# Kernel optimization log

Measured on AMD Instinct MI355X. Metric: run time of the kernel, lower is better.

The kernel has to match this reference:

```python
import jax, jax.numpy as jnp
import numpy as np

N = 10000
E = 160000
D = 512
EPS = 1e-5


def _lin_params(key, out_d, in_d, bias=True):
    k1, k2 = jax.random.split(key)
    s = 1.0 / np.sqrt(in_d)
    W = jax.random.uniform(k1, (out_d, in_d), jnp.float32, -s, s)
    if bias:
        b = jax.random.uniform(k2, (out_d,), jnp.float32, -s, s)
        return W, b
    return (W,)


def setup_inputs() -> dict:
    key = jax.random.key(0)
    ks = jax.random.split(key, 16)
    inp = {
        "x": jax.random.normal(ks[0], (N, D), jnp.float32),
        "edge_index": jax.random.randint(ks[1], (2, E), 0, N, jnp.int64),
    }
    ki = 2
    for l in range(3):
        Wp, bp = _lin_params(ks[ki], D, D); ki += 1
        Wl, bl = _lin_params(ks[ki], D, D); ki += 1
        (Wr,) = _lin_params(ks[ki], D, D, bias=False); ki += 1
        inp[f"Wp{l}"] = Wp; inp[f"bp{l}"] = bp
        inp[f"Wl{l}"] = Wl; inp[f"bl{l}"] = bl
        inp[f"Wr{l}"] = Wr
        if l < 2:  # ReLU+LayerNorm between convs
            inp[f"g{l}"] = jnp.ones((D,), jnp.float32)
            inp[f"be{l}"] = jnp.zeros((D,), jnp.float32)
    return inp


def _sage_conv(x, src, dst, Wp, bp, Wl, bl, Wr):
    # PyG SAGEConv with project=True: project+ReLU messages, mean-aggregate, lin_l + lin_r(root)
    h = jax.nn.relu(x @ Wp.T + bp)                      # [N, D] projected messages
    agg = jax.ops.segment_sum(h[src], dst, num_segments=N)   # gather + scatter-add
    cnt = jax.ops.segment_sum(jnp.ones((src.shape[0],), x.dtype), dst, num_segments=N)
    agg = agg / jnp.maximum(cnt, 1.0)[:, None]          # mean over incoming edges
    return agg @ Wl.T + bl + x @ Wr.T


def _relu_ln(x, g, b):
    x = jax.nn.relu(x)
    mu = jnp.mean(x, axis=-1, keepdims=True)
    var = jnp.mean(jnp.square(x - mu), axis=-1, keepdims=True)
    return (x - mu) * jax.lax.rsqrt(var + EPS) * g + b


def reference(x, edge_index,
              Wp0, bp0, Wl0, bl0, Wr0, g0, be0,
              Wp1, bp1, Wl1, bl1, Wr1, g1, be1,
              Wp2, bp2, Wl2, bl2, Wr2):
    src, dst = edge_index[0], edge_index[1]
    x = _sage_conv(x, src, dst, Wp0, bp0, Wl0, bl0, Wr0)
    x = _relu_ln(x, g0, be0)
    x = _sage_conv(x, src, dst, Wp1, bp1, Wl1, bl1, Wr1)
    x = _relu_ln(x, g1, be1)
    x = _sage_conv(x, src, dst, Wp2, bp2, Wl2, bl2, Wr2)
    return x
```

## Files before the change

### kernel.cpp

```cpp
#include <hip/hip_runtime.h>
#include <cstdint>

#define D 512
#define TM 128
#define TN 128
#define BK 32
#define CAP 64

typedef unsigned short u16;
typedef __bf16 bf16x8 __attribute__((ext_vector_type(8)));
typedef float f32x4 __attribute__((ext_vector_type(4)));

__device__ __forceinline__ float bf2f(u16 u) {
    unsigned int x = ((unsigned int)u) << 16;
    return __builtin_bit_cast(float, x);
}
__device__ __forceinline__ u16 f2bf(float f) {
    unsigned int x = __builtin_bit_cast(unsigned int, f);
    x += 0x7fffu + ((x >> 16) & 1u);
    return (u16)(x >> 16);
}

__device__ __forceinline__ void gload16(const u16* g, u16* l) {
    __builtin_amdgcn_global_load_lds(
        (const __attribute__((address_space(1))) void*)(uintptr_t)g,
        (__attribute__((address_space(3))) void*)(unsigned int)(uintptr_t)l,
        16, 0, 0);
}

__device__ __forceinline__ bool is_bf16(const u16* xraw) {
    int lane = threadIdx.x & 63;
    u16 u = xraw[2 * lane];
    int e = (u >> 7) & 0xFF;
    unsigned long long b = __ballot(e >= 110 && e <= 129);
    return __popcll(b) >= 32;
}
__device__ __forceinline__ bool is_i64(const int* eraw) {
    int lane = threadIdx.x & 63;
    unsigned long long b = __ballot(eraw[2 * lane + 1] == 0);
    return __popcll(b) >= 32;
}

__global__ __launch_bounds__(256) void convert_x(
    const void* __restrict__ src, u16* __restrict__ out)
{
    bool bf = is_bf16((const u16*)src);
    int i = (blockIdx.x * 256 + threadIdx.x) * 8;
    if (bf) {
        *(uint4*)(out + i) = *(const uint4*)((const u16*)src + i);
    } else {
        const float* f = (const float*)src + i;
        float4 a = *(const float4*)f;
        float4 b = *(const float4*)(f + 4);
        u16 r[8] = {f2bf(a.x), f2bf(a.y), f2bf(a.z), f2bf(a.w),
                    f2bf(b.x), f2bf(b.y), f2bf(b.z), f2bf(b.w)};
        *(uint4*)(out + i) = *(uint4*)r;
    }
}

struct Ptrs9  { const void* p[9];  };
struct Ptrs10 { const void* p[10]; };

__global__ __launch_bounds__(256) void convert_wb(
    Ptrs9 s, Ptrs10 v, u16* __restrict__ wout, float* __restrict__ vout,
    const u16* __restrict__ xraw)
{
    bool bf = is_bf16(xraw);
    int m = blockIdx.y;
    if (m < 9) {
        const void* src = s.p[m];
        u16* o = wout + (size_t)m * D * D;
        int i = (blockIdx.x * 256 + threadIdx.x) * 8;
        if (bf) {
            *(uint4*)(o + i) = *(const uint4*)((const u16*)src + i);
        } else {
            const float* f = (const float*)src + i;
            float4 a = *(const float4*)f;
            float4 b = *(const float4*)(f + 4);
            u16 r[8] = {f2bf(a.x), f2bf(a.y), f2bf(a.z), f2bf(a.w),
                        f2bf(b.x), f2bf(b.y), f2bf(b.z), f2bf(b.w)};
            *(uint4*)(o + i) = *(uint4*)r;
        }
    } else if (blockIdx.x == 0) {
        for (int b = 0; b < 10; b++) {
            const void* src = v.p[b];
            for (int j = threadIdx.x * 2; j < threadIdx.x * 2 + 2; j++) {
                float val = bf ? bf2f(((const u16*)src)[j]) : ((const float*)src)[j];
                vout[b * 512 + j] = val;
            }
        }
    }
}

__global__ void build_bucket(const int* __restrict__ eraw,
                             int* __restrict__ cnt, u16* __restrict__ bucket,
                             int E, int Nn)
{
    bool i64 = is_i64(eraw);
    int e = blockIdx.x * 256 + threadIdx.x;
    if (e < E) {
        int s, d;
        if (i64) { s = eraw[2 * e]; d = eraw[2 * (E + e)]; }
        else     { s = eraw[e];     d = eraw[E + e]; }
        s = min(max(s, 0), Nn - 1);
        d = min(max(d, 0), Nn - 1);
        int p = atomicAdd(&cnt[d], 1);
        if (p < CAP) bucket[(size_t)d * CAP + p] = (u16)s;
    }
}

template <int NPASS, bool RELU, bool FINAL>
__global__ __launch_bounds__(256) void gemm_bt(
    const u16* __restrict__ A0, const u16* __restrict__ B0,
    const u16* __restrict__ A1, const u16* __restrict__ B1,
    const float* __restrict__ bias, void* __restrict__ Cout,
    const u16* __restrict__ xraw, int M)
{
    __shared__ __align__(16) u16 sA[TM * BK];
    __shared__ __align__(16) u16 sB[TN * BK];

    const int t    = threadIdx.x;
    const int m0   = blockIdx.x * TM;
    const int n0   = blockIdx.y * TN;
    const int wave = t >> 6, lane = t & 63;
    const int wm   = wave >> 1, wn = wave & 1;
    const int lrow = lane & 15, quad = lane >> 4;

    const bool out_bf16 = FINAL ? is_bf16(xraw) : true;

    f32x4 acc[4][4];
#pragma unroll
    for (int i = 0; i < 4; i++)
#pragma unroll
        for (int j = 0; j < 4; j++)
#pragma unroll
            for (int r = 0; r < 4; r++) acc[i][j][r] = 0.f;

    const int cA  = (t & 3) * 8;
    const int rA0 = min(m0 + (t >> 2),      M - 1);
    const int rA1 = min(m0 + 64 + (t >> 2), M - 1);
    const int rB0 = n0 + (t >> 2);
    const int rB1 = n0 + 64 + (t >> 2);

#pragma unroll 1
    for (int p = 0; p < NPASS; p++) {
        const u16* A = p ? A1 : A0;
        const u16* B = p ? B1 : B0;
        const u16* gA0 = A + (size_t)rA0 * D + cA;
        const u16* gA1 = A + (size_t)rA1 * D + cA;
        const u16* gB0 = B + (size_t)rB0 * D + cA;
        const u16* gB1 = B + (size_t)rB1 * D + cA;

#pragma unroll 1
        for (int k0 = 0; k0 < D; k0 += BK) {
            gload16(gA0 + k0, &sA[(size_t)t * 8]);
            gload16(gA1 + k0, &sA[(size_t)(t + 256) * 8]);
            gload16(gB0 + k0, &sB[(size_t)t * 8]);
            gload16(gB1 + k0, &sB[(size_t)(t + 256) * 8]);
            __syncthreads();

            bf16x8 af[4], bfr[4];
#pragma unroll
            for (int mi = 0; mi < 4; mi++)
                af[mi] = *(const bf16x8*)&sA[(wm * 64 + mi * 16 + lrow) * BK + quad * 8];
#pragma unroll
            for (int ni = 0; ni < 4; ni++)
                bfr[ni] = *(const bf16x8*)&sB[(wn * 64 + ni * 16 + lrow) * BK + quad * 8];
#pragma unroll
            for (int mi = 0; mi < 4; mi++)
#pragma unroll
                for (int ni = 0; ni < 4; ni++)
                    acc[mi][ni] = __builtin_amdgcn_mfma_f32_16x16x32_bf16(
                        af[mi], bfr[ni], acc[mi][ni], 0, 0, 0);
            __syncthreads();
        }
    }

#pragma unroll
    for (int ni = 0; ni < 4; ni++) {
        int col = n0 + wn * 64 + ni * 16 + lrow;
        float bv = bias[col];
#pragma unroll
        for (int mi = 0; mi < 4; mi++) {
            int row0 = m0 + wm * 64 + mi * 16 + quad * 4;
#pragma unroll
            for (int r = 0; r < 4; r++) {
                int row = row0 + r;
                if (row < M) {
                    float v = acc[mi][ni][r] + bv;
                    if (RELU) v = fmaxf(v, 0.f);
                    if (!FINAL || out_bf16)
                        ((u16*)Cout)[(size_t)row * D + col] = f2bf(v);
                    else
                        ((float*)Cout)[(size_t)row * D + col] = v;
                }
            }
        }
    }
}

__global__ __launch_bounds__(256) void aggregate(
    const u16* __restrict__ h, const int* __restrict__ cnt,
    const u16* __restrict__ bucket, u16* __restrict__ agg, int M)
{
    const int w = threadIdx.x >> 6, lane = threadIdx.x & 63;
    const int n = blockIdx.x * 4 + w;

    __shared__ u16 sidx[4][CAP];
    int deg = 0, dd = 0;
    if (n < M) {
        deg = cnt[n];
        dd  = min(deg, CAP);
        if (lane < dd) sidx[w][lane] = bucket[(size_t)n * CAP + lane];
    }
    __syncthreads();
    if (n >= M) return;

    float a[8] = {0.f, 0.f, 0.f, 0.f, 0.f, 0.f, 0.f, 0.f};
    int i = 0;
    for (; i + 4 <= dd; i += 4) {
        uint4 v0 = *(const uint4*)(h + (size_t)sidx[w][i]     * D + lane * 8);
        uint4 v1 = *(const uint4*)(h + (size_t)sidx[w][i + 1] * D + lane * 8);
        uint4 v2 = *(const uint4*)(h + (size_t)sidx[w][i + 2] * D + lane * 8);
        uint4 v3 = *(const uint4*)(h + (size_t)sidx[w][i + 3] * D + lane * 8);
        const unsigned int* u0 = (const unsigned int*)&v0;
        const unsigned int* u1 = (const unsigned int*)&v1;
        const unsigned int* u2 = (const unsigned int*)&v2;
        const unsigned int* u3 = (const unsigned int*)&v3;
#pragma unroll
        for (int j = 0; j < 4; j++) {
            a[2 * j]     += bf2f((u16)(u0[j] & 0xffffu)) + bf2f((u16)(u1[j] & 0xffffu))
                          + bf2f((u16)(u2[j] & 0xffffu)) + bf2f((u16)(u3[j] & 0xffffu));
            a[2 * j + 1] += bf2f((u16)(u0[j] >> 16)) + bf2f((u16)(u1[j] >> 16))
                          + bf2f((u16)(u2[j] >> 16)) + bf2f((u16)(u3[j] >> 16));
        }
    }
    for (; i < dd; i++) {
        uint4 v0 = *(const uint4*)(h + (size_t)sidx[w][i] * D + lane * 8);
        const unsigned int* u0 = (const unsigned int*)&v0;
#pragma unroll
        for (int j = 0; j < 4; j++) {
            a[2 * j]     += bf2f((u16)(u0[j] & 0xffffu));
            a[2 * j + 1] += bf2f((u16)(u0[j] >> 16));
        }
    }

    float inv = 1.f / fmaxf((float)deg, 1.f);
    u16 r[8];
#pragma unroll
    for (int j = 0; j < 8; j++) r[j] = f2bf(a[j] * inv);
    *(uint4*)(agg + (size_t)n * D + lane * 8) = *(uint4*)r;
}

__global__ __launch_bounds__(256) void relu_ln(
    const u16* __restrict__ y, const float* __restrict__ g, const float* __restrict__ be,
    u16* __restrict__ out, int M)
{
    const int row  = blockIdx.x * 4 + (threadIdx.x >> 6);
    const int lane = threadIdx.x & 63;
    if (row >= M) return;

    typedef short s16x8 __attribute__((ext_vector_type(8)));
    s16x8 v = *(const s16x8*)(y + (size_t)row * D + lane * 8);
    float f[8], s = 0.f, s2 = 0.f;
#pragma unroll
    for (int i = 0; i < 8; i++) {
        float x = bf2f((u16)v[i]);
        x = fmaxf(x, 0.f);
        f[i] = x; s += x; s2 += x * x;
    }
#pragma unroll
    for (int off = 32; off >= 1; off >>= 1) {
        s  += __shfl_xor(s, off);
        s2 += __shfl_xor(s2, off);
    }
    float mean = s * (1.f / 512.f);
    float var  = s2 * (1.f / 512.f) - mean * mean;
    float rstd = rsqrtf(var + 1e-5f);

    s16x8 res;
#pragma unroll
    for (int i = 0; i < 8; i++) {
        float o = (f[i] - mean) * rstd * g[lane * 8 + i] + be[lane * 8 + i];
        res[i] = (short)f2bf(o);
    }
    *(s16x8*)(out + (size_t)row * D + lane * 8) = res;
}

extern "C" void kernel_launch(void* const* d_in, const int* in_sizes, int n_in,
                              void* d_out, int out_size, void* d_ws, size_t ws_size,
                              hipStream_t stream)
{
    const int M = in_sizes[0] / D;
    const int E = in_sizes[1] / 2;
    const void* xraw = d_in[0];
    const int*  eraw = (const int*)d_in[1];

    const void *Wp[3], *bp[3], *Wl[3], *bl[3], *Wr[3], *g[2], *be[2];
    int idx = 2;
    for (int l = 0; l < 3; l++) {
        Wp[l] = d_in[idx++]; bp[l] = d_in[idx++];
        Wl[l] = d_in[idx++]; bl[l] = d_in[idx++];
        Wr[l] = d_in[idx++];
        if (l < 2) { g[l] = d_in[idx++]; be[l] = d_in[idx++]; }
    }

    char* w = (char*)d_ws;
    auto alloc = [&](size_t bytes) { void* p = w; w += (bytes + 255) & ~(size_t)255; return p; };
    u16*   xb     = (u16*)  alloc((size_t)M * D * 2);
    u16*   h      = (u16*)  alloc((size_t)M * D * 2);
    u16*   agg    = (u16*)  alloc((size_t)M * D * 2);
    u16*   Wb     = (u16*)  alloc((size_t)9 * D * D * 2);
    float* vecf   = (float*)alloc((size_t)10 * 512 * 4);
    int*   cnt    = (int*)  alloc((size_t)M * 4);
    u16*   bucket = (u16*)  alloc((size_t)M * CAP * 2);

    convert_x<<<dim3(M * D / (256 * 8)), dim3(256), 0, stream>>>(xraw, xb);

    Ptrs9 mats;
    const void* morder[9] = {Wp[0], Wl[0], Wr[0], Wp[1], Wl[1], Wr[1], Wp[2], Wl[2], Wr[2]};
    for (int i = 0; i < 9; i++) mats.p[i] = morder[i];
    Ptrs10 vecs;
    const void* vorder[10] = {bp[0], bl[0], g[0], be[0], bp[1], bl[1], g[1], be[1], bp[2], bl[2]};
    for (int i = 0; i < 10; i++) vecs.p[i] = vorder[i];
    convert_wb<<<dim3(D * D / (256 * 8), 10), dim3(256), 0, stream>>>(
        mats, vecs, Wb, vecf, (const u16*)xraw);

    hipMemsetAsync(cnt, 0, (size_t)M * 4, stream);
    build_bucket<<<dim3((E + 255) / 256), dim3(256), 0, stream>>>(eraw, cnt, bucket, E, M);

    const u16* WM[9]; for (int i = 0; i < 9; i++) WM[i] = Wb + (size_t)i * D * D;
    const float* VB[10]; for (int i = 0; i < 10; i++) VB[i] = vecf + (size_t)i * 512;

    u16* yb = (u16*)d_out;
    dim3 gg((M + TM - 1) / TM, D / TN);
    const u16* xin = xb;
    for (int l = 0; l < 3; l++) {
        gemm_bt<1, true, false><<<gg, dim3(256), 0, stream>>>(
            xin, WM[l * 3 + 0], xin, WM[l * 3 + 0], VB[l * 4 + 0], h, (const u16*)xraw, M);
        aggregate<<<dim3((M + 3) / 4), dim3(256), 0, stream>>>(h, cnt, bucket, agg, M);
        if (l < 2) {
            gemm_bt<2, false, false><<<gg, dim3(256), 0, stream>>>(
                agg, WM[l * 3 + 1], xin, WM[l * 3 + 2], VB[l * 4 + 1], yb, (const u16*)xraw, M);
            relu_ln<<<dim3((M + 3) / 4), dim3(256), 0, stream>>>(
                yb, VB[l * 4 + 2], VB[l * 4 + 3], xb, M);
            xin = xb;
        } else {
            gemm_bt<2, false, true><<<gg, dim3(256), 0, stream>>>(
                agg, WM[l * 3 + 1], xin, WM[l * 3 + 2], VB[l * 4 + 1], d_out, (const u16*)xraw, M);
        }
    }
}
```

Baseline: 381.0 us.

## Fuse whole pipeline into one persistent kernel with grid barriers

Replaces the separate conversion, bucket-build, GEMM, aggregate and LayerNorm launches with a single persistent kernel that uses a software grid barrier between phases. The GEMM also switches from direct global-to-LDS loads to register-prefetched double buffering, and the aggregation keeps neighbor indices in registers and broadcasts them with shuffles instead of staging them in shared memory. The intent is to remove launch overhead and inter-kernel gaps. In exchange, each barrier costs global atomics and spinning, and the grid size is fixed by the GEMM tile count. Correctness relies on every block being co-resident, which the launch does not guarantee, so the barrier can deadlock.

```diff
diff --git a/kernel.cpp b/kernel.cpp
--- a/kernel.cpp
+++ b/kernel.cpp
@@ -19,13 +19,6 @@
     unsigned int x = __builtin_bit_cast(unsigned int, f);
     x += 0x7fffu + ((x >> 16) & 1u);
     return (u16)(x >> 16);
-}
-
-__device__ __forceinline__ void gload16(const u16* g, u16* l) {
-    __builtin_amdgcn_global_load_lds(
-        (const __attribute__((address_space(1))) void*)(uintptr_t)g,
-        (__attribute__((address_space(3))) void*)(unsigned int)(uintptr_t)l,
-        16, 0, 0);
 }
 
 __device__ __forceinline__ bool is_bf16(const u16* xraw) {
@@ -41,92 +34,94 @@
     return __popcll(b) >= 32;
 }
 
-__global__ __launch_bounds__(256) void convert_x(
-    const void* __restrict__ src, u16* __restrict__ out)
+struct Args {
+    const u16* xraw; const int* eraw;
+    const void* W[9];
+    const void* V[10];
+    u16* xb; u16* h; u16* agg; u16* Wb; float* vecf;
+    int* cnt; u16* bucket; int* bar;
+    void* dout;
+    int M, E, NGRP;
+};
+
+__device__ __forceinline__ void grid_sync(int* cnt, int* gen, int nb) {
+    __syncthreads();
+    if (threadIdx.x == 0) {
+        int g0 = __hip_atomic_load(gen, __ATOMIC_RELAXED, __HIP_MEMORY_SCOPE_AGENT);
+        __threadfence();
+        int prev = __hip_atomic_fetch_add(cnt, 1, __ATOMIC_RELAXED, __HIP_MEMORY_SCOPE_AGENT);
+        if (prev == nb - 1) {
+            __hip_atomic_store(cnt, 0, __ATOMIC_RELAXED, __HIP_MEMORY_SCOPE_AGENT);
+            __hip_atomic_fetch_add(gen, 1, __ATOMIC_RELAXED, __HIP_MEMORY_SCOPE_AGENT);
+        } else {
+            while (__hip_atomic_load(gen, __ATOMIC_RELAXED, __HIP_MEMORY_SCOPE_AGENT) == g0)
+                __builtin_amdgcn_s_sleep(2);
+        }
+        __threadfence();
+    }
+    __syncthreads();
+}
+
+__device__ void phase0(const Args& a, bool bf, bool i64) {
+    const int gt = blockIdx.x * 256 + threadIdx.x;
+    const int gs = gridDim.x * 256;
+
+    const int nx = a.M * D / 8;
+    for (int i = gt; i < nx; i += gs) {
+        if (bf) {
+            *(uint4*)(a.xb + i * 8) = *(const uint4*)(a.xraw + i * 8);
+        } else {
+            const float* f = (const float*)a.xraw + i * 8;
+            float4 p = *(const float4*)f, q = *(const float4*)(f + 4);
+            u16 r[8] = {f2bf(p.x), f2bf(p.y), f2bf(p.z), f2bf(p.w),
+                        f2bf(q.x), f2bf(q.y), f2bf(q.z), f2bf(q.w)};
+            *(uint4*)(a.xb + i * 8) = *(uint4*)r;
+        }
+    }
+    for (int i = gt; i < 9 * 32768; i += gs) {
+        int m = i >> 15, j = i & 32767;
+        const void* src = a.W[m];
+        u16* o = a.Wb + (size_t)m * D * D + j * 8;
+        if (bf) {
+            *(uint4*)o = *(const uint4*)((const u16*)src + j * 8);
+        } else {
+            const float* f = (const float*)src + j * 8;
+            float4 p = *(const float4*)f, q = *(const float4*)(f + 4);
+            u16 r[8] = {f2bf(p.x), f2bf(p.y), f2bf(p.z), f2bf(p.w),
+                        f2bf(q.x), f2bf(q.y), f2bf(q.z), f2bf(q.w)};
+            *(uint4*)o = *(uint4*)r;
+        }
+    }
+    if (blockIdx.x < 10) {
+        const void* src = a.V[blockIdx.x];
+        for (int j = threadIdx.x * 2; j < threadIdx.x * 2 + 2; j++) {
+            a.vecf[blockIdx.x * 512 + j] =
+                bf ? bf2f(((const u16*)src)[j]) : ((const float*)src)[j];
+        }
+    }
+    for (int e = gt; e < a.E; e += gs) {
+        int s, d;
+        if (i64) { s = a.eraw[2 * e]; d = a.eraw[2 * (a.E + e)]; }
+        else     { s = a.eraw[e];     d = a.eraw[a.E + e]; }
+        s = min(max(s, 0), a.M - 1);
+        d = min(max(d, 0), a.M - 1);
+        int p = atomicAdd(&a.cnt[d], 1);
+        if (p < CAP) a.bucket[(size_t)d * CAP + p] = (u16)s;
+    }
+}
+
+template <int NPASS, bool RELU, bool FINAL>
+__device__ void gemm_tile(const u16* __restrict__ A0, const u16* __restrict__ B0,
+                          const u16* __restrict__ A1, const u16* __restrict__ B1,
+                          const float* __restrict__ bias, void* __restrict__ Cout,
+                          int M, bool out_bf16, u16* sA, u16* sB)
 {
-    bool bf = is_bf16((const u16*)src);
-    int i = (blockIdx.x * 256 + threadIdx.x) * 8;
-    if (bf) {
-        *(uint4*)(out + i) = *(const uint4*)((const u16*)src + i);
-    } else {
-        const float* f = (const float*)src + i;
-        float4 a = *(const float4*)f;
-        float4 b = *(const float4*)(f + 4);
-        u16 r[8] = {f2bf(a.x), f2bf(a.y), f2bf(a.z), f2bf(a.w),
-                    f2bf(b.x), f2bf(b.y), f2bf(b.z), f2bf(b.w)};
-        *(uint4*)(out + i) = *(uint4*)r;
-    }
-}
-
-struct Ptrs9  { const void* p[9];  };
-struct Ptrs10 { const void* p[10]; };
-
-__global__ __launch_bounds__(256) void convert_wb(
-    Ptrs9 s, Ptrs10 v, u16* __restrict__ wout, float* __restrict__ vout,
-    const u16* __restrict__ xraw)
-{
-    bool bf = is_bf16(xraw);
-    int m = blockIdx.y;
-    if (m < 9) {
-        const void* src = s.p[m];
-        u16* o = wout + (size_t)m * D * D;
-        int i = (blockIdx.x * 256 + threadIdx.x) * 8;
-        if (bf) {
-            *(uint4*)(o + i) = *(const uint4*)((const u16*)src + i);
-        } else {
-            const float* f = (const float*)src + i;
-            float4 a = *(const float4*)f;
-            float4 b = *(const float4*)(f + 4);
-            u16 r[8] = {f2bf(a.x), f2bf(a.y), f2bf(a.z), f2bf(a.w),
-                        f2bf(b.x), f2bf(b.y), f2bf(b.z), f2bf(b.w)};
-            *(uint4*)(o + i) = *(uint4*)r;
-        }
-    } else if (blockIdx.x == 0) {
-        for (int b = 0; b < 10; b++) {
-            const void* src = v.p[b];
-            for (int j = threadIdx.x * 2; j < threadIdx.x * 2 + 2; j++) {
-                float val = bf ? bf2f(((const u16*)src)[j]) : ((const float*)src)[j];
-                vout[b * 512 + j] = val;
-            }
-        }
-    }
-}
-
-__global__ void build_bucket(const int* __restrict__ eraw,
-                             int* __restrict__ cnt, u16* __restrict__ bucket,
-                             int E, int Nn)
-{
-    bool i64 = is_i64(eraw);
-    int e = blockIdx.x * 256 + threadIdx.x;
-    if (e < E) {
-        int s, d;
-        if (i64) { s = eraw[2 * e]; d = eraw[2 * (E + e)]; }
-        else     { s = eraw[e];     d = eraw[E + e]; }
-        s = min(max(s, 0), Nn - 1);
-        d = min(max(d, 0), Nn - 1);
-        int p = atomicAdd(&cnt[d], 1);
-        if (p < CAP) bucket[(size_t)d * CAP + p] = (u16)s;
-    }
-}
-
-template <int NPASS, bool RELU, bool FINAL>
-__global__ __launch_bounds__(256) void gemm_bt(
-    const u16* __restrict__ A0, const u16* __restrict__ B0,
-    const u16* __restrict__ A1, const u16* __restrict__ B1,
-    const float* __restrict__ bias, void* __restrict__ Cout,
-    const u16* __restrict__ xraw, int M)
-{
-    __shared__ __align__(16) u16 sA[TM * BK];
-    __shared__ __align__(16) u16 sB[TN * BK];
-
     const int t    = threadIdx.x;
-    const int m0   = blockIdx.x * TM;
-    const int n0   = blockIdx.y * TN;
+    const int m0   = (blockIdx.x >> 2) * TM;
+    const int n0   = (blockIdx.x & 3) * TN;
     const int wave = t >> 6, lane = t & 63;
     const int wm   = wave >> 1, wn = wave & 1;
     const int lrow = lane & 15, quad = lane >> 4;
-
-    const bool out_bf16 = FINAL ? is_bf16(xraw) : true;
 
     f32x4 acc[4][4];
 #pragma unroll
@@ -142,38 +137,44 @@
     const int rB0 = n0 + (t >> 2);
     const int rB1 = n0 + 64 + (t >> 2);
 
+    uint4 va0 = *(const uint4*)(A0 + (size_t)rA0 * D + cA);
+    uint4 va1 = *(const uint4*)(A0 + (size_t)rA1 * D + cA);
+    uint4 vb0 = *(const uint4*)(B0 + (size_t)rB0 * D + cA);
+    uint4 vb1 = *(const uint4*)(B0 + (size_t)rB1 * D + cA);
+
 #pragma unroll 1
-    for (int p = 0; p < NPASS; p++) {
-        const u16* A = p ? A1 : A0;
-        const u16* B = p ? B1 : B0;
-        const u16* gA0 = A + (size_t)rA0 * D + cA;
-        const u16* gA1 = A + (size_t)rA1 * D + cA;
-        const u16* gB0 = B + (size_t)rB0 * D + cA;
-        const u16* gB1 = B + (size_t)rB1 * D + cA;
-
-#pragma unroll 1
-        for (int k0 = 0; k0 < D; k0 += BK) {
-            gload16(gA0 + k0, &sA[(size_t)t * 8]);
-            gload16(gA1 + k0, &sA[(size_t)(t + 256) * 8]);
-            gload16(gB0 + k0, &sB[(size_t)t * 8]);
-            gload16(gB1 + k0, &sB[(size_t)(t + 256) * 8]);
-            __syncthreads();
-
-            bf16x8 af[4], bfr[4];
-#pragma unroll
-            for (int mi = 0; mi < 4; mi++)
-                af[mi] = *(const bf16x8*)&sA[(wm * 64 + mi * 16 + lrow) * BK + quad * 8];
+    for (int kk = 0; kk < NPASS * D; kk += BK) {
+        __syncthreads();
+        *(uint4*)&sA[t * 8]         = va0;
+        *(uint4*)&sA[(t + 256) * 8] = va1;
+        *(uint4*)&sB[t * 8]         = vb0;
+        *(uint4*)&sB[(t + 256) * 8] = vb1;
+        __syncthreads();
+
+        const int kn = kk + BK;
+        if (kn < NPASS * D) {
+            const u16* A = (NPASS == 2 && kn >= D) ? A1 : A0;
+            const u16* B = (NPASS == 2 && kn >= D) ? B1 : B0;
+            const int k = kn & (D - 1);
+            va0 = *(const uint4*)(A + (size_t)rA0 * D + k + cA);
+            va1 = *(const uint4*)(A + (size_t)rA1 * D + k + cA);
+            vb0 = *(const uint4*)(B + (size_t)rB0 * D + k + cA);
+            vb1 = *(const uint4*)(B + (size_t)rB1 * D + k + cA);
+        }
+
+        bf16x8 af[4], bfr[4];
+#pragma unroll
+        for (int mi = 0; mi < 4; mi++)
+            af[mi] = *(const bf16x8*)&sA[(wm * 64 + mi * 16 + lrow) * BK + quad * 8];
+#pragma unroll
+        for (int ni = 0; ni < 4; ni++)
+            bfr[ni] = *(const bf16x8*)&sB[(wn * 64 + ni * 16 + lrow) * BK + quad * 8];
+#pragma unroll
+        for (int mi = 0; mi < 4; mi++)
 #pragma unroll
             for (int ni = 0; ni < 4; ni++)
-                bfr[ni] = *(const bf16x8*)&sB[(wn * 64 + ni * 16 + lrow) * BK + quad * 8];
-#pragma unroll
-            for (int mi = 0; mi < 4; mi++)
-#pragma unroll
-                for (int ni = 0; ni < 4; ni++)
-                    acc[mi][ni] = __builtin_amdgcn_mfma_f32_16x16x32_bf16(
-                        af[mi], bfr[ni], acc[mi][ni], 0, 0, 0);
-            __syncthreads();
-        }
+                acc[mi][ni] = __builtin_amdgcn_mfma_f32_16x16x32_bf16(
+                    af[mi], bfr[ni], acc[mi][ni], 0, 0, 0);
     }
 
 #pragma unroll
@@ -199,92 +200,130 @@
     }
 }
 
-__global__ __launch_bounds__(256) void aggregate(
-    const u16* __restrict__ h, const int* __restrict__ cnt,
-    const u16* __restrict__ bucket, u16* __restrict__ agg, int M)
+__device__ void agg_phase(const u16* __restrict__ h, const int* __restrict__ cnt,
+                          const u16* __restrict__ bucket, u16* __restrict__ agg,
+                          int M, int ngrp)
 {
-    const int w = threadIdx.x >> 6, lane = threadIdx.x & 63;
-    const int n = blockIdx.x * 4 + w;
-
-    __shared__ u16 sidx[4][CAP];
-    int deg = 0, dd = 0;
-    if (n < M) {
-        deg = cnt[n];
-        dd  = min(deg, CAP);
-        if (lane < dd) sidx[w][lane] = bucket[(size_t)n * CAP + lane];
-    }
-    __syncthreads();
-    if (n >= M) return;
-
-    float a[8] = {0.f, 0.f, 0.f, 0.f, 0.f, 0.f, 0.f, 0.f};
-    int i = 0;
-    for (; i + 4 <= dd; i += 4) {
-        uint4 v0 = *(const uint4*)(h + (size_t)sidx[w][i]     * D + lane * 8);
-        uint4 v1 = *(const uint4*)(h + (size_t)sidx[w][i + 1] * D + lane * 8);
-        uint4 v2 = *(const uint4*)(h + (size_t)sidx[w][i + 2] * D + lane * 8);
-        uint4 v3 = *(const uint4*)(h + (size_t)sidx[w][i + 3] * D + lane * 8);
-        const unsigned int* u0 = (const unsigned int*)&v0;
-        const unsigned int* u1 = (const unsigned int*)&v1;
-        const unsigned int* u2 = (const unsigned int*)&v2;
-        const unsigned int* u3 = (const unsigned int*)&v3;
-#pragma unroll
-        for (int j = 0; j < 4; j++) {
-            a[2 * j]     += bf2f((u16)(u0[j] & 0xffffu)) + bf2f((u16)(u1[j] & 0xffffu))
-                          + bf2f((u16)(u2[j] & 0xffffu)) + bf2f((u16)(u3[j] & 0xffffu));
-            a[2 * j + 1] += bf2f((u16)(u0[j] >> 16)) + bf2f((u16)(u1[j] >> 16))
-                          + bf2f((u16)(u2[j] >> 16)) + bf2f((u16)(u3[j] >> 16));
-        }
-    }
-    for (; i < dd; i++) {
-        uint4 v0 = *(const uint4*)(h + (size_t)sidx[w][i] * D + lane * 8);
-        const unsigned int* u0 = (const unsigned int*)&v0;
-#pragma unroll
-        for (int j = 0; j < 4; j++) {
-            a[2 * j]     += bf2f((u16)(u0[j] & 0xffffu));
-            a[2 * j + 1] += bf2f((u16)(u0[j] >> 16));
-        }
-    }
-
-    float inv = 1.f / fmaxf((float)deg, 1.f);
-    u16 r[8];
-#pragma unroll
-    for (int j = 0; j < 8; j++) r[j] = f2bf(a[j] * inv);
-    *(uint4*)(agg + (size_t)n * D + lane * 8) = *(uint4*)r;
-}
-
-__global__ __launch_bounds__(256) void relu_ln(
-    const u16* __restrict__ y, const float* __restrict__ g, const float* __restrict__ be,
-    u16* __restrict__ out, int M)
+    const int wave = threadIdx.x >> 6, lane = threadIdx.x & 63;
+    for (int grp = blockIdx.x; grp < ngrp; grp += gridDim.x) {
+        int n = grp * 4 + wave;
+        if (n >= M) continue;
+        int deg = cnt[n];
+        int dd  = min(deg, CAP);
+        int myi = (lane < dd) ? (int)bucket[(size_t)n * CAP + lane] : 0;
+
+        float a[8] = {0.f, 0.f, 0.f, 0.f, 0.f, 0.f, 0.f, 0.f};
+        int i = 0;
+        for (; i + 4 <= dd; i += 4) {
+            int s0 = __shfl(myi, i), s1 = __shfl(myi, i + 1);
+            int s2 = __shfl(myi, i + 2), s3 = __shfl(myi, i + 3);
+            uint4 v0 = *(const uint4*)(h + (size_t)s0 * D + lane * 8);
+            uint4 v1 = *(const uint4*)(h + (size_t)s1 * D + lane * 8);
+            uint4 v2 = *(const uint4*)(h + (size_t)s2 * D + lane * 8);
+            uint4 v3 = *(const uint4*)(h + (size_t)s3 * D + lane * 8);
+            const unsigned int* u0 = (const unsigned int*)&v0;
+            const unsigned int* u1 = (const unsigned int*)&v1;
+            const unsigned int* u2 = (const unsigned int*)&v2;
+            const unsigned int* u3 = (const unsigned int*)&v3;
+#pragma unroll
+            for (int j = 0; j < 4; j++) {
+                a[2 * j]     += bf2f((u16)(u0[j] & 0xffffu)) + bf2f((u16)(u1[j] & 0xffffu))
+                              + bf2f((u16)(u2[j] & 0xffffu)) + bf2f((u16)(u3[j] & 0xffffu));
+                a[2 * j + 1] += bf2f((u16)(u0[j] >> 16)) + bf2f((u16)(u1[j] >> 16))
+                              + bf2f((u16)(u2[j] >> 16)) + bf2f((u16)(u3[j] >> 16));
+            }
+        }
+        for (; i < dd; i++) {
+            int s0 = __shfl(myi, i);
+            uint4 v0 = *(const uint4*)(h + (size_t)s0 * D + lane * 8);
+            const unsigned int* u0 = (const unsigned int*)&v0;
+#pragma unroll
+            for (int j = 0; j < 4; j++) {
+                a[2 * j]     += bf2f((u16)(u0[j] & 0xffffu));
+                a[2 * j + 1] += bf2f((u16)(u0[j] >> 16));
+            }
+        }
+        float inv = 1.f / fmaxf((float)deg, 1.f);
+        u16 r[8];
+#pragma unroll
+        for (int j = 0; j < 8; j++) r[j] = f2bf(a[j] * inv);
+        *(uint4*)(agg + (size_t)n * D + lane * 8) = *(uint4*)r;
+    }
+}
+
+__device__ void ln_phase(const u16* __restrict__ y, const float* __restrict__ g,
+                         const float* __restrict__ be, u16* __restrict__ out,
+                         int M, int ngrp)
 {
-    const int row  = blockIdx.x * 4 + (threadIdx.x >> 6);
-    const int lane = threadIdx.x & 63;
-    if (row >= M) return;
-
-    typedef short s16x8 __attribute__((ext_vector_type(8)));
-    s16x8 v = *(const s16x8*)(y + (size_t)row * D + lane * 8);
-    float f[8], s = 0.f, s2 = 0.f;
-#pragma unroll
-    for (int i = 0; i < 8; i++) {
-        float x = bf2f((u16)v[i]);
-        x = fmaxf(x, 0.f);
-        f[i] = x; s += x; s2 += x * x;
-    }
-#pragma unroll
-    for (int off = 32; off >= 1; off >>= 1) {
-        s  += __shfl_xor(s, off);
-        s2 += __shfl_xor(s2, off);
-    }
-    float mean = s * (1.f / 512.f);
-    float var  = s2 * (1.f / 512.f) - mean * mean;
-    float rstd = rsqrtf(var + 1e-5f);
-
-    s16x8 res;
-#pragma unroll
-    for (int i = 0; i < 8; i++) {
-        float o = (f[i] - mean) * rstd * g[lane * 8 + i] + be[lane * 8 + i];
-        res[i] = (short)f2bf(o);
-    }
-    *(s16x8*)(out + (size_t)row * D + lane * 8) = res;
+    const int wave = threadIdx.x >> 6, lane = threadIdx.x & 63;
+    for (int grp = blockIdx.x; grp < ngrp; grp += gridDim.x) {
+        int row = grp * 4 + wave;
+        if (row >= M) continue;
+        typedef short s16x8 __attribute__((ext_vector_type(8)));
+        s16x8 v = *(const s16x8*)(y + (size_t)row * D + lane * 8);
+        float f[8], s = 0.f, s2 = 0.f;
+#pragma unroll
+        for (int i = 0; i < 8; i++) {
+            float x = bf2f((u16)v[i]);
+            x = fmaxf(x, 0.f);
+            f[i] = x; s += x; s2 += x * x;
+        }
+#pragma unroll
+        for (int off = 32; off >= 1; off >>= 1) {
+            s  += __shfl_xor(s, off);
+            s2 += __shfl_xor(s2, off);
+        }
+        float mean = s * (1.f / 512.f);
+        float var  = s2 * (1.f / 512.f) - mean * mean;
+        float rstd = rsqrtf(var + 1e-5f);
+        s16x8 res;
+#pragma unroll
+        for (int i = 0; i < 8; i++) {
+            float o = (f[i] - mean) * rstd * g[lane * 8 + i] + be[lane * 8 + i];
+            res[i] = (short)f2bf(o);
+        }
+        *(s16x8*)(out + (size_t)row * D + lane * 8) = res;
+    }
+}
+
+__global__ __launch_bounds__(256, 2) void mega(Args a) {
+    __shared__ __align__(16) u16 sA[TM * BK];
+    __shared__ __align__(16) u16 sB[TN * BK];
+
+    const bool bf  = is_bf16(a.xraw);
+    const bool i64 = is_i64(a.eraw);
+    int* bcnt = a.bar;
+    int* bgen = a.bar + 1;
+    const int NB = gridDim.x;
+
+    phase0(a, bf, i64);
+    grid_sync(bcnt, bgen, NB);
+
+    const u16* xin = a.xb;
+    u16* yb = (u16*)a.dout;
+    for (int l = 0; l < 3; l++) {
+        const u16* Wp = a.Wb + (size_t)(l * 3 + 0) * D * D;
+        const u16* Wl = a.Wb + (size_t)(l * 3 + 1) * D * D;
+        const u16* Wr = a.Wb + (size_t)(l * 3 + 2) * D * D;
+        const float* bp = a.vecf + (l * 4 + 0) * 512;
+        const float* bl = a.vecf + (l * 4 + 1) * 512;
+
+        gemm_tile<1, true, false>(xin, Wp, xin, Wp, bp, a.h, a.M, true, sA, sB);
+        grid_sync(bcnt, bgen, NB);
+        agg_phase(a.h, a.cnt, a.bucket, a.agg, a.M, a.NGRP);
+        grid_sync(bcnt, bgen, NB);
+        if (l < 2) {
+            gemm_tile<2, false, false>(a.agg, Wl, xin, Wr, bl, yb, a.M, true, sA, sB);
+            grid_sync(bcnt, bgen, NB);
+            const float* g  = a.vecf + (l * 4 + 2) * 512;
+            const float* be = a.vecf + (l * 4 + 3) * 512;
+            ln_phase(yb, g, be, a.xb, a.M, a.NGRP);
+            grid_sync(bcnt, bgen, NB);
+            xin = a.xb;
+        } else {
+            gemm_tile<2, false, true>(a.agg, Wl, xin, Wr, bl, a.dout, a.M, bf, sA, sB);
+        }
+    }
 }
 
 extern "C" void kernel_launch(void* const* d_in, const int* in_sizes, int n_in,
@@ -293,61 +332,41 @@
 {
     const int M = in_sizes[0] / D;
     const int E = in_sizes[1] / 2;
-    const void* xraw = d_in[0];
-    const int*  eraw = (const int*)d_in[1];
-
-    const void *Wp[3], *bp[3], *Wl[3], *bl[3], *Wr[3], *g[2], *be[2];
-    int idx = 2;
-    for (int l = 0; l < 3; l++) {
-        Wp[l] = d_in[idx++]; bp[l] = d_in[idx++];
-        Wl[l] = d_in[idx++]; bl[l] = d_in[idx++];
-        Wr[l] = d_in[idx++];
-        if (l < 2) { g[l] = d_in[idx++]; be[l] = d_in[idx++]; }
+
+    Args a;
+    a.xraw = (const u16*)d_in[0];
+    a.eraw = (const int*)d_in[1];
+    {
+        int idx = 2;
+        for (int l = 0; l < 3; l++) {
+            a.W[l * 3 + 0] = d_in[idx++];
+            a.V[l * 4 + 0] = d_in[idx++];
+            a.W[l * 3 + 1] = d_in[idx++];
+            a.V[l * 4 + 1] = d_in[idx++];
+            a.W[l * 3 + 2] = d_in[idx++];
+            if (l < 2) {
+                a.V[l * 4 + 2] = d_in[idx++];
+                a.V[l * 4 + 3] = d_in[idx++];
+            }
+        }
     }
 
     char* w = (char*)d_ws;
     auto alloc = [&](size_t bytes) { void* p = w; w += (bytes + 255) & ~(size_t)255; return p; };
-    u16*   xb     = (u16*)  alloc((size_t)M * D * 2);
-    u16*   h      = (u16*)  alloc((size_t)M * D * 2);
-    u16*   agg    = (u16*)  alloc((size_t)M * D * 2);
-    u16*   Wb     = (u16*)  alloc((size_t)9 * D * D * 2);
-    float* vecf   = (float*)alloc((size_t)10 * 512 * 4);
-    int*   cnt    = (int*)  alloc((size_t)M * 4);
-    u16*   bucket = (u16*)  alloc((size_t)M * CAP * 2);
-
-    convert_x<<<dim3(M * D / (256 * 8)), dim3(256), 0, stream>>>(xraw, xb);
-
-    Ptrs9 mats;
-    const void* morder[9] = {Wp[0], Wl[0], Wr[0], Wp[1], Wl[1], Wr[1], Wp[2], Wl[2], Wr[2]};
-    for (int i = 0; i < 9; i++) mats.p[i] = morder[i];
-    Ptrs10 vecs;
-    const void* vorder[10] = {bp[0], bl[0], g[0], be[0], bp[1], bl[1], g[1], be[1], bp[2], bl[2]};
-    for (int i = 0; i < 10; i++) vecs.p[i] = vorder[i];
-    convert_wb<<<dim3(D * D / (256 * 8), 10), dim3(256), 0, stream>>>(
-        mats, vecs, Wb, vecf, (const u16*)xraw);
-
-    hipMemsetAsync(cnt, 0, (size_t)M * 4, stream);
-    build_bucket<<<dim3((E + 255) / 256), dim3(256), 0, stream>>>(eraw, cnt, bucket, E, M);
-
-    const u16* WM[9]; for (int i = 0; i < 9; i++) WM[i] = Wb + (size_t)i * D * D;
-    const float* VB[10]; for (int i = 0; i < 10; i++) VB[i] = vecf + (size_t)i * 512;
-
-    u16* yb = (u16*)d_out;
-    dim3 gg((M + TM - 1) / TM, D / TN);
-    const u16* xin = xb;
-    for (int l = 0; l < 3; l++) {
-        gemm_bt<1, true, false><<<gg, dim3(256), 0, stream>>>(
-            xin, WM[l * 3 + 0], xin, WM[l * 3 + 0], VB[l * 4 + 0], h, (const u16*)xraw, M);
-        aggregate<<<dim3((M + 3) / 4), dim3(256), 0, stream>>>(h, cnt, bucket, agg, M);
-        if (l < 2) {
-            gemm_bt<2, false, false><<<gg, dim3(256), 0, stream>>>(
-                agg, WM[l * 3 + 1], xin, WM[l * 3 + 2], VB[l * 4 + 1], yb, (const u16*)xraw, M);
-            relu_ln<<<dim3((M + 3) / 4), dim3(256), 0, stream>>>(
-                yb, VB[l * 4 + 2], VB[l * 4 + 3], xb, M);
-            xin = xb;
-        } else {
-            gemm_bt<2, false, true><<<gg, dim3(256), 0, stream>>>(
-                agg, WM[l * 3 + 1], xin, WM[l * 3 + 2], VB[l * 4 + 1], d_out, (const u16*)xraw, M);
-        }
-    }
-}
+    a.xb     = (u16*)  alloc((size_t)M * D * 2);
+    a.h      = (u16*)  alloc((size_t)M * D * 2);
+    a.agg    = (u16*)  alloc((size_t)M * D * 2);
+    a.Wb     = (u16*)  alloc((size_t)9 * D * D * 2);
+    a.vecf   = (float*)alloc((size_t)10 * 512 * 4);
+    size_t cnt_rounded = ((size_t)M * 4 + 255) & ~(size_t)255;
+    a.cnt    = (int*)  alloc((size_t)M * 4);
+    a.bar    = (int*)  alloc(256);
+    a.bucket = (u16*)  alloc((size_t)M * CAP * 2);
+    a.dout   = d_out;
+    a.M = M; a.E = E; a.NGRP = (M + 3) / 4;
+
+    hipMemsetAsync(a.cnt, 0, cnt_rounded + 256, stream);
+
+    const int NT = ((M + TM - 1) / TM) * 4;
+    mega<<<dim3(NT), dim3(256), 0, stream>>>(a);
+}
```

Result: slower. 848.8 us (+122.8%).
